# Kernel tuning notes

Measured on AMD Instinct MI355X. Metric: run time of the kernel, lower is better.

## Reference

```python
import jax, jax.numpy as jnp
import numpy as np


def setup_inputs() -> dict:
    key = jax.random.key(0)
    ks = jax.random.split(key, 7)
    B, P, D = 4, 2048, 1024
    s = 1.0 / np.sqrt(D)
    return {
        "x":  jax.random.normal(ks[0], (B, P, D), dtype=jnp.float32),
        "Wq": jax.random.normal(ks[1], (D, D), dtype=jnp.float32) * s,
        "bq": jnp.zeros((D,), dtype=jnp.float32),
        "Wk": jax.random.normal(ks[2], (D, D), dtype=jnp.float32) * s,
        "bk": jnp.zeros((D,), dtype=jnp.float32),
        "Wv": jax.random.normal(ks[3], (D, D), dtype=jnp.float32) * s,
        "bv": jnp.zeros((D,), dtype=jnp.float32),
    }


def reference(x, Wq, bq, Wk, bk, Wv, bv):
    # x: [B, P, D]; Linear uses W stored torch-style [out, in]: y = x @ W.T + b
    b, p, d = x.shape
    q = jnp.einsum("bpd,ed->bpe", x, Wq) + bq
    k = jnp.einsum("bpd,ed->bpe", x, Wk) + bk
    v = jnp.einsum("bpd,ed->bpe", x, Wv) + bv
    attn = jnp.einsum("bqd,bkd->bqk", q, k)  # [B, P, P]
    causal = jnp.triu(jnp.ones((p, p), dtype=bool), k=1)  # True above diagonal
    attn = jnp.where(causal, -jnp.inf, attn)
    attn = attn / jnp.sqrt(jnp.asarray(d, dtype=attn.dtype))
    scores = jax.nn.softmax(attn, axis=-1)
    # dropout is identity in eval/deterministic mode
    return jnp.einsum("bqk,bkd->bqd", scores, v)
```

## Files before the change

### kernel.cpp

```cpp
#include <hip/hip_runtime.h>
#include <hip/hip_bf16.h>


typedef __attribute__((ext_vector_type(8))) short bf16x8;
typedef __attribute__((ext_vector_type(4))) float f32x4;

__device__ __forceinline__ unsigned short f2bf(float f) {
    union { float f; unsigned u; } v; v.f = f;
    unsigned r = v.u + 0x7FFF + ((v.u >> 16) & 1);
    return (unsigned short)(r >> 16);
}

__device__ __forceinline__ void gload_lds16(const unsigned short* g, unsigned short* l) {
    __builtin_amdgcn_global_load_lds(
        (const __attribute__((address_space(1))) unsigned int*)g,
        (__attribute__((address_space(3))) unsigned int*)l, 16, 0, 0);
}

__global__ void convert_kernel(const float* __restrict__ x,  const float* __restrict__ wq,
                               const float* __restrict__ wk, const float* __restrict__ wv,
                               const float* __restrict__ bq, const float* __restrict__ bk,
                               const float* __restrict__ bv,
                               unsigned short* __restrict__ xb, unsigned short* __restrict__ wqkvb,
                               float* __restrict__ bqkv, float* __restrict__ lsum) {
    long t = (long)blockIdx.x * blockDim.x + threadIdx.x;
    long idx = t * 4;
    const float* src; unsigned short* dst; long off;
    if      (idx <  8388608) { src = x;  dst = xb;            off = idx;            }
    else if (idx <  9437184) { src = wq; dst = wqkvb;         off = idx -  8388608; }
    else if (idx < 10485760) { src = wk; dst = wqkvb+1048576; off = idx -  9437184; }
    else if (idx < 11534336) { src = wv; dst = wqkvb+2097152; off = idx - 10485760; }
    else return;
    float4 v = *(const float4*)(src + off);
    ushort4 o = make_ushort4(f2bf(v.x), f2bf(v.y), f2bf(v.z), f2bf(v.w));
    *(ushort4*)(dst + off) = o;
    if (t < 768) {
        long o2 = t * 4;
        float4 b;
        if      (o2 < 1024) b = *(const float4*)(bq + o2);
        else if (o2 < 2048) b = *(const float4*)(bk + o2 - 1024);
        else                b = *(const float4*)(bv + o2 - 2048);
        *(float4*)(bqkv + o2) = b;
    }
    if (t >= 1024 && t < 3072) {
        float4 z = make_float4(0.f, 0.f, 0.f, 0.f);
        *(float4*)(lsum + (t - 1024) * 4) = z;
    }
}

__device__ __forceinline__ void stage(const unsigned short* gA, long lda,
                                      const unsigned short* gB, long ldb,
                                      unsigned short* As, unsigned short* Bs,
                                      int w, int k0) {
#pragma unroll
    for (int s = 0; s < 4; ++s) {
        gload_lds16(gA + k0 + (long)(s * 8) * lda, &As[(w * 32 + s * 8) * 64]);
        gload_lds16(gB + k0 + (long)(s * 8) * ldb, &Bs[(w * 32 + s * 8) * 64]);
    }
}

template<bool SWAP>
__device__ __forceinline__ void mfma_tile(const unsigned short* As, const unsigned short* Bs,
                                          int wr, int wc, int ln, int pr0, int pr1,
                                          f32x4 (&acc)[4][4]) {
#pragma unroll
    for (int kk = 0; kk < 2; ++kk) {
        const int pr = kk ? pr1 : pr0;
        bf16x8 af[4], bfr[4];
#pragma unroll
        for (int i = 0; i < 4; ++i)
            af[i] = *(const bf16x8*)(&As[(wr + i * 16 + ln) * 64 + pr]);
#pragma unroll
        for (int j = 0; j < 4; ++j)
            bfr[j] = *(const bf16x8*)(&Bs[(wc + j * 16 + ln) * 64 + pr]);
#pragma unroll
        for (int i = 0; i < 4; ++i)
#pragma unroll
            for (int j = 0; j < 4; ++j)
                acc[i][j] = SWAP
                    ? __builtin_amdgcn_mfma_f32_16x16x32_bf16(bfr[j], af[i], acc[i][j], 0, 0, 0)
                    : __builtin_amdgcn_mfma_f32_16x16x32_bf16(af[i], bfr[j], acc[i][j], 0, 0, 0);
    }
}

template<bool SWAP>
__device__ __forceinline__ void kloop_db(const unsigned short* gA, long lda,
                                         const unsigned short* gB, long ldb,
                                         unsigned short* As0, unsigned short* Bs0,
                                         unsigned short* As1, unsigned short* Bs1,
                                         int w, int lane, int Keff, f32x4 (&acc)[4][4]) {
    const int q  = lane >> 4;
    const int ln = lane & 15;
    const int wr = (w >> 1) * 64;
    const int wc = (w & 1) * 64;
    const int pr0 = ((q)     ^ (ln & 7)) * 8;
    const int pr1 = ((q + 4) ^ (ln & 7)) * 8;
    stage(gA, lda, gB, ldb, As0, Bs0, w, 0);
    __syncthreads();
    for (int k0 = 0; k0 < Keff; k0 += 128) {
        stage(gA, lda, gB, ldb, As1, Bs1, w, k0 + 64);
        mfma_tile<SWAP>(As0, Bs0, wr, wc, ln, pr0, pr1, acc);
        __syncthreads();
        if (k0 + 128 < Keff)
            stage(gA, lda, gB, ldb, As0, Bs0, w, k0 + 128);
        mfma_tile<SWAP>(As1, Bs1, wr, wc, ln, pr0, pr1, acc);
        __syncthreads();
    }
}

__global__ __launch_bounds__(256, 2)
void gemm_qkv(const unsigned short* __restrict__ X,
              const unsigned short* __restrict__ W,
              unsigned short* __restrict__ QK,
              unsigned short* __restrict__ VT,
              const float* __restrict__ bias) {
    const int n0 = blockIdx.x * 128;
    const int m0 = blockIdx.y * 128;
    __shared__ __align__(16) unsigned short As0[128 * 64], Bs0[128 * 64];
    __shared__ __align__(16) unsigned short As1[128 * 64], Bs1[128 * 64];
    const int tid = threadIdx.x, lane = tid & 63, w = tid >> 6;
    const int q = lane >> 4, ln = lane & 15;
    const int wr = (w >> 1) * 64, wc = (w & 1) * 64;
    const int srow = lane >> 3, sc = (lane & 7) ^ srow;
    const unsigned short* gA = X + (long)(m0 + w * 32 + srow) * 1024 + sc * 8;
    const unsigned short* gB = W + (long)(n0 + w * 32 + srow) * 1024 + sc * 8;
    f32x4 acc[4][4] = {};
    if (n0 >= 2048) {
        kloop_db<false>(gA, 1024, gB, 1024, As0, Bs0, As1, Bs1, w, lane, 1024, acc);
#pragma unroll
        for (int j = 0; j < 4; ++j) {
            const int e = n0 - 2048 + wc + j * 16 + ln;
            const float bc = bias[n0 + wc + j * 16 + ln];
#pragma unroll
            for (int i = 0; i < 4; ++i) {
                const int m = m0 + wr + i * 16 + q * 4;
                ushort4 o = make_ushort4(f2bf(acc[i][j][0] + bc), f2bf(acc[i][j][1] + bc),
                                         f2bf(acc[i][j][2] + bc), f2bf(acc[i][j][3] + bc));
                *(ushort4*)(VT + (long)e * 8192 + m) = o;
            }
        }
    } else {
        kloop_db<true>(gA, 1024, gB, 1024, As0, Bs0, As1, Bs1, w, lane, 1024, acc);
#pragma unroll
        for (int j = 0; j < 4; ++j) {
            const float4 bc = *(const float4*)(bias + n0 + wc + j * 16 + q * 4);
#pragma unroll
            for (int i = 0; i < 4; ++i) {
                const int m = m0 + wr + i * 16 + ln;
                const int n = n0 + wc + j * 16 + q * 4;
                ushort4 o = make_ushort4(f2bf(acc[i][j][0] + bc.x), f2bf(acc[i][j][1] + bc.y),
                                         f2bf(acc[i][j][2] + bc.z), f2bf(acc[i][j][3] + bc.w));
                *(ushort4*)(QK + (long)m * 2048 + n) = o;
            }
        }
    }
}

__global__ __launch_bounds__(256, 2)
void gemm_scores(const unsigned short* __restrict__ QK,
                 unsigned short* __restrict__ P,
                 float* __restrict__ lsum) {
    const int t = blockIdx.x;
    int i = (int)((sqrtf(8.0f * t + 1.0f) - 1.0f) * 0.5f);
    while ((i + 1) * (i + 2) / 2 <= t) ++i;
    while (i * (i + 1) / 2 > t) --i;
    const int j = t - i * (i + 1) / 2;
    const int m0 = i * 128, n0 = j * 128, z = blockIdx.y;
    const unsigned short* Qz = QK + (long)z * 2048 * 2048;
    const unsigned short* Kz = Qz + 1024;
    unsigned short* Pz = P + (long)z * 2048 * 2048;
    float* lz = lsum + z * 2048;

    __shared__ __align__(16) unsigned short As0[128 * 64], Bs0[128 * 64];
    __shared__ __align__(16) unsigned short As1[128 * 64], Bs1[128 * 64];
    const int tid = threadIdx.x, lane = tid & 63, w = tid >> 6;
    const int q = lane >> 4, ln = lane & 15;
    const int wr = (w >> 1) * 64, wc = (w & 1) * 64;
    const int srow = lane >> 3, sc = (lane & 7) ^ srow;
    const unsigned short* gA = Qz + (long)(m0 + w * 32 + srow) * 2048 + sc * 8;
    const unsigned short* gB = Kz + (long)(n0 + w * 32 + srow) * 2048 + sc * 8;
    f32x4 acc[4][4] = {};
    kloop_db<true>(gA, 2048, gB, 2048, As0, Bs0, As1, Bs1, w, lane, 1024, acc);

    const float scale = 0.03125f;
#pragma unroll
    for (int i2 = 0; i2 < 4; ++i2) {
        const int m = m0 + wr + i2 * 16 + ln;
        float rs = 0.f;
#pragma unroll
        for (int j2 = 0; j2 < 4; ++j2) {
            const int n = n0 + wc + j2 * 16 + q * 4;
            float p0 = (n     <= m) ? __expf(acc[i2][j2][0] * scale) : 0.f;
            float p1 = (n + 1 <= m) ? __expf(acc[i2][j2][1] * scale) : 0.f;
            float p2 = (n + 2 <= m) ? __expf(acc[i2][j2][2] * scale) : 0.f;
            float p3 = (n + 3 <= m) ? __expf(acc[i2][j2][3] * scale) : 0.f;
            rs += (p0 + p1) + (p2 + p3);
            ushort4 o = make_ushort4(f2bf(p0), f2bf(p1), f2bf(p2), f2bf(p3));
            *(ushort4*)(Pz + (long)m * 2048 + n) = o;
        }
        rs += __shfl_xor(rs, 16); rs += __shfl_xor(rs, 32);
        if (lane < 16) atomicAdd(&lz[m], rs);
    }
}

__global__ __launch_bounds__(256, 2)
void gemm_pv(const unsigned short* __restrict__ P,
             const unsigned short* __restrict__ VT,
             const float* __restrict__ lsum,
             float* __restrict__ out) {
    const int L  = blockIdx.x;
    const int ph = L >> 8;
    const int c  = L & 255;
    const int z  = c >> 6;
    const int r  = c & 63;
    const int mh = r >> 3;
    const int nt = r & 7;
    const int mt = ph ? 15 - mh : mh;
    const int m0 = mt * 128, n0 = nt * 128;
    const int Keff = m0 + 128;
    const unsigned short* Pz = P + (long)z * 2048 * 2048;
    const unsigned short* Vz = VT + (long)z * 2048;
    const float* lz = lsum + z * 2048;

    __shared__ __align__(16) unsigned short As0[128 * 64], Bs0[128 * 64];
    __shared__ __align__(16) unsigned short As1[128 * 64], Bs1[128 * 64];
    const int tid = threadIdx.x, lane = tid & 63, w = tid >> 6;
    const int q = lane >> 4, ln = lane & 15;
    const int wr = (w >> 1) * 64, wc = (w & 1) * 64;
    const int srow = lane >> 3, sc = (lane & 7) ^ srow;
    const unsigned short* gA = Pz + (long)(m0 + w * 32 + srow) * 2048 + sc * 8;
    const unsigned short* gB = Vz + (long)(n0 + w * 32 + srow) * 8192 + sc * 8;
    f32x4 acc[4][4] = {};
    kloop_db<true>(gA, 2048, gB, 8192, As0, Bs0, As1, Bs1, w, lane, Keff, acc);

#pragma unroll
    for (int i2 = 0; i2 < 4; ++i2) {
        const int m = m0 + wr + i2 * 16 + ln;
        const float inv = 1.0f / lz[m];
#pragma unroll
        for (int j2 = 0; j2 < 4; ++j2) {
            const int n = n0 + wc + j2 * 16 + q * 4;
            f32x4 o;
            o[0] = acc[i2][j2][0] * inv; o[1] = acc[i2][j2][1] * inv;
            o[2] = acc[i2][j2][2] * inv; o[3] = acc[i2][j2][3] * inv;
            __builtin_nontemporal_store(o, (f32x4*)(out + (long)(z * 2048 + m) * 1024 + n));
        }
    }
}

extern "C" void kernel_launch(void* const* d_in, const int* in_sizes, int n_in,
                              void* d_out, int out_size, void* d_ws, size_t ws_size,
                              hipStream_t stream) {
    const float* x  = (const float*)d_in[0];
    const float* Wq = (const float*)d_in[1];
    const float* bq = (const float*)d_in[2];
    const float* Wk = (const float*)d_in[3];
    const float* bk = (const float*)d_in[4];
    const float* Wv = (const float*)d_in[5];
    const float* bv = (const float*)d_in[6];
    float* out = (float*)d_out;

    char* ws = (char*)d_ws;
    unsigned short* xb    = (unsigned short*)ws; ws += (long)8192 * 1024 * 2;
    unsigned short* wqkvb = (unsigned short*)ws; ws += (long)3072 * 1024 * 2;
    float*          bqkv  = (float*)ws;          ws += (long)3072 * 4;
    float*          lsum  = (float*)ws;          ws += (long)8192 * 4;
    unsigned short* QKb   = (unsigned short*)ws; ws += (long)8192 * 2048 * 2;
    unsigned short* VTb   = (unsigned short*)ws; ws += (long)1024 * 8192 * 2;
    unsigned short* Pb    = (unsigned short*)ws; ws += (long)4 * 2048 * 2048 * 2;

    hipLaunchKernelGGL(convert_kernel, dim3(11264), dim3(256), 0, stream,
                       x, Wq, Wk, Wv, bq, bk, bv, xb, wqkvb, bqkv, lsum);

    hipLaunchKernelGGL(gemm_qkv, dim3(24, 64, 1), dim3(256), 0, stream,
                       xb, wqkvb, QKb, VTb, bqkv);

    hipLaunchKernelGGL(gemm_scores, dim3(136, 4, 1), dim3(256), 0, stream,
                       QKb, Pb, lsum);

    hipLaunchKernelGGL(gemm_pv, dim3(512, 1, 1), dim3(256), 0, stream,
                       Pb, VTb, lsum, out);
}
```

Measured before the change: 242.5 us.

## Shrink score GEMM tiles to 64x128 with custom causal tile mapping

The scores kernel now uses 64-row by 128-column tiles instead of 128x128, with a new triangular index mapping that enumerates 64-row strips, and it doubles the grid to 272 blocks per batch. Staging and MFMA helpers are specialised for the smaller A tile, and launch bounds are raised to 3 blocks per CU. The aim is better occupancy and load balance on the causal triangle, and less wasted work on diagonal tiles. In exchange, each block reuses less data per loaded tile and the kernel issues more global loads overall.

```diff
diff --git a/kernel.cpp b/kernel.cpp
--- a/kernel.cpp
+++ b/kernel.cpp
@@ -156,35 +156,82 @@
     }
 }
 
-__global__ __launch_bounds__(256, 2)
+__device__ __forceinline__ void stage64(const unsigned short* gA, const unsigned short* gB,
+                                        unsigned short* As, unsigned short* Bs,
+                                        int w, int k0) {
+    gload_lds16(gA + k0,                     &As[(w * 8) * 64]);
+    gload_lds16(gA + k0 + (long)32 * 2048,   &As[(32 + w * 8) * 64]);
+#pragma unroll
+    for (int s = 0; s < 4; ++s)
+        gload_lds16(gB + k0 + (long)(s * 32) * 2048, &Bs[(s * 32 + w * 8) * 64]);
+}
+
+__device__ __forceinline__ void mfma_tile64(const unsigned short* As, const unsigned short* Bs,
+                                            int wr, int wc, int ln, int pr0, int pr1,
+                                            f32x4 (&acc)[2][4]) {
+#pragma unroll
+    for (int kk = 0; kk < 2; ++kk) {
+        const int pr = kk ? pr1 : pr0;
+        bf16x8 af[2], bfr[4];
+#pragma unroll
+        for (int i = 0; i < 2; ++i)
+            af[i] = *(const bf16x8*)(&As[(wr + i * 16 + ln) * 64 + pr]);
+#pragma unroll
+        for (int j = 0; j < 4; ++j)
+            bfr[j] = *(const bf16x8*)(&Bs[(wc + j * 16 + ln) * 64 + pr]);
+#pragma unroll
+        for (int i = 0; i < 2; ++i)
+#pragma unroll
+            for (int j = 0; j < 4; ++j)
+                acc[i][j] = __builtin_amdgcn_mfma_f32_16x16x32_bf16(bfr[j], af[i], acc[i][j], 0, 0, 0);
+    }
+}
+
+__global__ __launch_bounds__(256, 3)
 void gemm_scores(const unsigned short* __restrict__ QK,
                  unsigned short* __restrict__ P,
                  float* __restrict__ lsum) {
     const int t = blockIdx.x;
-    int i = (int)((sqrtf(8.0f * t + 1.0f) - 1.0f) * 0.5f);
-    while ((i + 1) * (i + 2) / 2 <= t) ++i;
-    while (i * (i + 1) / 2 > t) --i;
-    const int j = t - i * (i + 1) / 2;
-    const int m0 = i * 128, n0 = j * 128, z = blockIdx.y;
+    int g = (int)((sqrtf(4.0f * t + 1.0f) - 1.0f) * 0.5f);
+    while ((g + 1) * (g + 2) <= t) ++g;
+    while (g * (g + 1) > t) --g;
+    const int r  = t - g * (g + 1);
+    const int gp = g + 1;
+    const int i64 = 2 * g + (r >= gp ? 1 : 0);
+    const int j   = (r >= gp) ? (r - gp) : r;
+    const int m0 = i64 * 64, n0 = j * 128, z = blockIdx.y;
     const unsigned short* Qz = QK + (long)z * 2048 * 2048;
     const unsigned short* Kz = Qz + 1024;
     unsigned short* Pz = P + (long)z * 2048 * 2048;
     float* lz = lsum + z * 2048;
 
-    __shared__ __align__(16) unsigned short As0[128 * 64], Bs0[128 * 64];
-    __shared__ __align__(16) unsigned short As1[128 * 64], Bs1[128 * 64];
+    __shared__ __align__(16) unsigned short As0[64 * 64], Bs0[128 * 64];
+    __shared__ __align__(16) unsigned short As1[64 * 64], Bs1[128 * 64];
     const int tid = threadIdx.x, lane = tid & 63, w = tid >> 6;
     const int q = lane >> 4, ln = lane & 15;
-    const int wr = (w >> 1) * 64, wc = (w & 1) * 64;
+    const int wr = (w >> 1) * 32, wc = (w & 1) * 64;
     const int srow = lane >> 3, sc = (lane & 7) ^ srow;
-    const unsigned short* gA = Qz + (long)(m0 + w * 32 + srow) * 2048 + sc * 8;
-    const unsigned short* gB = Kz + (long)(n0 + w * 32 + srow) * 2048 + sc * 8;
-    f32x4 acc[4][4] = {};
-    kloop_db<true>(gA, 2048, gB, 2048, As0, Bs0, As1, Bs1, w, lane, 1024, acc);
+    const int pr0 = ((q)     ^ (ln & 7)) * 8;
+    const int pr1 = ((q + 4) ^ (ln & 7)) * 8;
+    const unsigned short* gA = Qz + (long)(m0 + w * 8 + srow) * 2048 + sc * 8;
+    const unsigned short* gB = Kz + (long)(n0 + w * 8 + srow) * 2048 + sc * 8;
+    f32x4 acc[2][4] = {};
+
+    stage64(gA, gB, As0, Bs0, w, 0);
+    __syncthreads();
+    for (int k0 = 0; k0 < 1024; k0 += 128) {
+        stage64(gA, gB, As1, Bs1, w, k0 + 64);
+        mfma_tile64(As0, Bs0, wr, wc, ln, pr0, pr1, acc);
+        __syncthreads();
+        if (k0 + 128 < 1024)
+            stage64(gA, gB, As0, Bs0, w, k0 + 128);
+        mfma_tile64(As1, Bs1, wr, wc, ln, pr0, pr1, acc);
+        __syncthreads();
+    }
 
     const float scale = 0.03125f;
 #pragma unroll
-    for (int i2 = 0; i2 < 4; ++i2) {
+    for (int i2 = 0; i2 < 2; ++i2) {
         const int m = m0 + wr + i2 * 16 + ln;
         float rs = 0.f;
 #pragma unroll
@@ -275,7 +322,7 @@
     hipLaunchKernelGGL(gemm_qkv, dim3(24, 64, 1), dim3(256), 0, stream,
                        xb, wqkvb, QKb, VTb, bqkv);
 
-    hipLaunchKernelGGL(gemm_scores, dim3(136, 4, 1), dim3(256), 0, stream,
+    hipLaunchKernelGGL(gemm_scores, dim3(272, 4, 1), dim3(256), 0, stream,
                        QKb, Pb, lsum);
 
     hipLaunchKernelGGL(gemm_pv, dim3(512, 1, 1), dim3(256), 0, stream,
```

Result: faster. 230.0 us (-5.1%).
